# Performance work log

Hardware: AMD Instinct MI355X
Metric: run time of the kernel (lower is better)

## Reference

```python
import math
import jax, jax.numpy as jnp
import numpy as np

IN_FEATURES = 4096
OUT_FEATURES = 4096
BLOCK_SIZE = 256
N_TOKENS = 8192


def _butterfly_layout(out_blocks, in_blocks, butterfly_size):
    # sum of log2(n) butterfly factors with all-ones 2x2 twiddles:
    # block (o, i) is active iff o == i or o == i ^ 2^k for some factor k
    log_n = int(math.log2(butterfly_size))
    idx = np.arange(butterfly_size)
    layout = np.zeros((butterfly_size, butterfly_size), dtype=bool)
    layout[idx, idx] = True
    for k in range(log_n):
        layout[idx ^ (1 << k), idx] = True
    if out_blocks > butterfly_size:
        layout = np.tile(layout, (out_blocks // butterfly_size, 1))
    if in_blocks > butterfly_size:
        layout = np.tile(layout, (1, in_blocks // butterfly_size))
    return layout


def _flat_indices(layout):
    # For each output block, flat indices into [num_in_blocks * active_blocks_per_input]
    # selecting which per-input weight blocks are summed (embedding_bag mode='sum').
    num_out, num_in = layout.shape
    abpi = int(layout.sum(0)[0])
    abpo = int(layout.sum(1)[0])
    rank = np.cumsum(layout, axis=0) - 1  # rank of output o among active outputs of input i
    o_idx, i_idx = np.nonzero(layout)     # row-major -> grouped by output block
    flat = i_idx * abpi + rank[o_idx, i_idx]
    return flat.reshape(num_out, abpo).astype(np.int32), abpi


def setup_inputs() -> dict:
    key = jax.random.key(0)
    k1, k2 = jax.random.split(key)
    in_blocks = IN_FEATURES // BLOCK_SIZE
    out_blocks = OUT_FEATURES // BLOCK_SIZE
    butterfly_size = min(IN_FEATURES, OUT_FEATURES) // BLOCK_SIZE  # 16
    layout = _butterfly_layout(out_blocks, in_blocks, butterfly_size)
    flat_idx, abpi = _flat_indices(layout)  # abpi = log2(16)+1 = 5
    std = math.sqrt(2.0 / (5 * min(IN_FEATURES, OUT_FEATURES)))
    weight = jax.random.normal(k1, (IN_FEATURES, abpi, BLOCK_SIZE), dtype=jnp.float32) * std
    x = jax.random.normal(k2, (N_TOKENS, IN_FEATURES), dtype=jnp.float32)
    return {"x": x, "weight": weight, "flat_indices": jnp.asarray(flat_idx)}


def reference(x, weight, flat_indices):
    # x: [B, in_features]; weight: [in_features, abpi, block_size]
    in_features, abpi, bs = weight.shape
    num_in = in_features // bs
    B = x.shape[0]
    xb = x.reshape(B, num_in, bs)                  # [B, g, k]
    w = weight.reshape(num_in, bs, abpi, bs)       # [g, k, a, o]
    # per-input-block partial output blocks: [g, a, B, o]
    blocks = jnp.einsum('bgk,gkao->gabo', xb, w)
    blocks = blocks.reshape(num_in * abpi, B, bs)
    # gather + sum active blocks per output block (embedding_bag mode='sum')
    out_blocks = blocks[flat_indices].sum(axis=1)  # [num_out_blocks, B, bs]
    out = jnp.transpose(out_blocks, (1, 0, 2)).reshape(B, -1)  # [B, out_features]
    return out
```

## Files before the change

kernel.cpp:

```cpp
#include <hip/hip_runtime.h>
#include <stdint.h>

#define N_TOK 8192
#define IN_F 4096
#define OUT_F 4096
#define BS 256
#define ABPI 5
#define NFLAT 80

typedef __attribute__((ext_vector_type(8))) short short8;
typedef __attribute__((ext_vector_type(4))) float floatx4;
typedef __attribute__((ext_vector_type(4))) unsigned short ushort4v;

__device__ __forceinline__ unsigned short f2bf(float f) {
  union { float f; unsigned int u; } v; v.f = f;
  unsigned int r = v.u + 0x7FFFu + ((v.u >> 16) & 1u);
  return (unsigned short)(r >> 16);
}

__device__ __forceinline__ void async16(const void* g, void* l) {
  __builtin_amdgcn_global_load_lds((const __attribute__((address_space(1))) void*)g,
                                   (__attribute__((address_space(3))) void*)l, 16, 0, 0);
}

__global__ void cvt_x_kernel(const float4* __restrict__ x, ushort4v* __restrict__ xb) {
  int idx = blockIdx.x * 256 + threadIdx.x;
  const int stride = 2048 * 256;
  #pragma unroll
  for (int i = 0; i < 16; ++i, idx += stride) {
    float4 a = x[idx];
    ushort4v o;
    o[0] = f2bf(a.x); o[1] = f2bf(a.y); o[2] = f2bf(a.z); o[3] = f2bf(a.w);
    xb[idx] = o;
  }
}

__global__ void cvt_w_kernel(const float* __restrict__ w, unsigned short* __restrict__ wt) {
  __shared__ unsigned short tile[64][68];
  int b = blockIdx.x;
  int fi = b >> 4;
  int t  = b & 15;
  int k0 = (t >> 2) * 64, o0 = (t & 3) * 64;
  int g = fi / ABPI, a = fi % ABPI;
  int tid = threadIdx.x;
  int tr = tid >> 4, tc = tid & 15;
  #pragma unroll
  for (int i = 0; i < 4; ++i) {
    int k = k0 + i * 16 + tr;
    const float* src = w + (size_t)(g * 256 + k) * (ABPI * BS) + a * BS + o0 + tc * 4;
    float4 v = *(const float4*)src;
    tile[tc * 4 + 0][i * 16 + tr] = f2bf(v.x);
    tile[tc * 4 + 1][i * 16 + tr] = f2bf(v.y);
    tile[tc * 4 + 2][i * 16 + tr] = f2bf(v.z);
    tile[tc * 4 + 3][i * 16 + tr] = f2bf(v.w);
  }
  __syncthreads();
  #pragma unroll
  for (int i = 0; i < 4; ++i) {
    int o = i * 16 + tr;
    unsigned short* dst = wt + (size_t)fi * (BS * BS) + (size_t)(o0 + o) * BS + k0 + tc * 4;
    *(ushort4v*)dst = *(const ushort4v*)&tile[o][tc * 4];
  }
}


#define BM 256
#define BN 256
#define BK 64
#define ABYTES 32768
#define BUFBYTES 65536
#define SMEM_TOTAL 131072

#define SB() __builtin_amdgcn_sched_barrier(0)
#define PRIO1() __builtin_amdgcn_s_setprio(1)
#define PRIO0() __builtin_amdgcn_s_setprio(0)
#define BARRIER() __builtin_amdgcn_s_barrier()
#define LGKM0() do { asm volatile("s_waitcnt lgkmcnt(0)" ::: "memory"); SB(); } while (0)

__device__ __forceinline__ void ld_half_A(const char* p, int c0, int c1, short8 (&af)[4][2]) {
  #pragma unroll
  for (int mt = 0; mt < 4; ++mt) {
    const char* q = p + mt * 2048;
    af[mt][0] = *(const short8*)(q + c0);
    af[mt][1] = *(const short8*)(q + c1);
  }
}

__device__ __forceinline__ void ld_pair_B(const char* p, int c0, int c1, short8 (&bf)[2][2]) {
  #pragma unroll
  for (int nt = 0; nt < 2; ++nt) {
    const char* q = p + nt * 2048;
    bf[nt][0] = *(const short8*)(q + c0);
    bf[nt][1] = *(const short8*)(q + c1);
  }
}

__device__ __forceinline__ void mma16(const short8 (&af)[4][2], const short8 (&bf)[2][2],
                                      floatx4 (&acc)[8][4], int mb, int nb) {
  #pragma unroll
  for (int mt = 0; mt < 4; ++mt)
    #pragma unroll
    for (int nt = 0; nt < 2; ++nt) {
      acc[mb + mt][nb + nt] =
          __builtin_amdgcn_mfma_f32_16x16x32_bf16(af[mt][0], bf[nt][0], acc[mb + mt][nb + nt], 0, 0, 0);
      acc[mb + mt][nb + nt] =
          __builtin_amdgcn_mfma_f32_16x16x32_bf16(af[mt][1], bf[nt][1], acc[mb + mt][nb + nt], 0, 0, 0);
    }
}

#define KTILE(Ab, Bb, Bsd, uB, uA2, STB, STA, END)                              \
  do {                                                                          \
                     \
    if (STB) { async16(pB0 + (uB), (Bsd)         + tid16);                      \
               async16(pB1 + (uB), (Bsd) +  8192 + tid16); }                    \
    ld_half_A((Ab) + rAb,        c0, c1, af);                                   \
    ld_pair_B((Bb) + rBb,        c0, c1, bf01);                                 \
    ld_pair_B((Bb) + rBb + 4096, c0, c1, bf23);                                 \
    SB(); BARRIER(); LGKM0();                                                   \
    PRIO1(); mma16(af, bf01, acc, 0, 0); PRIO0();                               \
    BARRIER();                                                                  \
                                          \
    if (STB) { async16(pB2 + (uB), (Bsd) + 16384 + tid16);                      \
               async16(pB3 + (uB), (Bsd) + 24576 + tid16); }                    \
    SB(); BARRIER();                                                            \
    PRIO1(); mma16(af, bf23, acc, 0, 2); PRIO0();                               \
    BARRIER();                                                                  \
     \
    if (STA) { async16(pA0 + (uA2), (Ab)         + tid16);                      \
               async16(pA2 + (uA2), (Ab) + 16384 + tid16); }                    \
    ld_half_A((Ab) + rAb + 8192, c0, c1, af);                                   \
    SB(); BARRIER(); LGKM0();                                                   \
    PRIO1(); mma16(af, bf23, acc, 4, 2); PRIO0();                               \
    BARRIER();                                                                  \
                                            \
    if (STA) { async16(pA1 + (uA2), (Ab) +  8192 + tid16);                      \
               async16(pA3 + (uA2), (Ab) + 24576 + tid16); }                    \
    SB(); BARRIER();                                                            \
    PRIO1(); mma16(af, bf01, acc, 4, 0); PRIO0();                               \
    if ((END) == 2)      { asm volatile("s_waitcnt vmcnt(4)" ::: "memory");     \
                           SB(); BARRIER(); }                                   \
    else if ((END) == 1) { asm volatile("s_waitcnt vmcnt(0)" ::: "memory");     \
                           SB(); BARRIER(); }                                   \
  } while (0)

__global__ __launch_bounds__(512, 2)
void bfly_gemm(const unsigned short* __restrict__ xb,
               const unsigned short* __restrict__ wt,
               const int* __restrict__ fidx,
               float* __restrict__ out)
{
  extern __shared__ __align__(16) char smem[];
  char* const b0A = smem;
  char* const b0B = b0A + ABYTES;
  char* const b1A = smem + BUFBYTES;
  char* const b1B = b1A + ABYTES;

  const int tid = threadIdx.x;
  const int bx  = blockIdx.x;
  const int swz = (bx & 7) * 64 + (bx >> 3);
  const int ob  = swz >> 5;
  const int mt0 = swz & 31;
  const int m0  = mt0 * BM;
  const int n0g = ob * 256;

  int wbase[ABPI], gcol[ABPI];
  #pragma unroll
  for (int s = 0; s < ABPI; ++s) {
    int fi = __builtin_amdgcn_readfirstlane(fidx[ob * ABPI + s]);
    wbase[s] = fi * (BS * BS);
    gcol[s]  = (fi / ABPI) * BS;
  }

  const int sr = tid >> 3;
  const int sc = tid & 7;
  const int lc = sc ^ (sr & 7);
  const int tid16 = tid * 16;
  const unsigned short* pA0 = xb + (size_t)(m0 +   0 + sr) * IN_F + lc * 8;
  const unsigned short* pA1 = xb + (size_t)(m0 +  64 + sr) * IN_F + lc * 8;
  const unsigned short* pA2 = xb + (size_t)(m0 + 128 + sr) * IN_F + lc * 8;
  const unsigned short* pA3 = xb + (size_t)(m0 + 192 + sr) * IN_F + lc * 8;
  const unsigned short* pB0 = wt + (  0 + sr) * BS + lc * 8;
  const unsigned short* pB1 = wt + ( 64 + sr) * BS + lc * 8;
  const unsigned short* pB2 = wt + (128 + sr) * BS + lc * 8;
  const unsigned short* pB3 = wt + (192 + sr) * BS + lc * 8;

  const int lane = tid & 63;
  const int wv   = tid >> 6;
  const int wm   = (wv >> 2) * 128;
  const int wn   = (wv & 3) * 64;
  const int lrow = lane & 15;
  const int quad = lane >> 4;
  const int rAb  = (wm + lrow) * 128;
  const int rBb  = (wn + lrow) * 128;
  const int c0   = ((quad)     ^ (lrow & 7)) * 16;
  const int c1   = ((quad + 4) ^ (lrow & 7)) * 16;

  short8 af[4][2], bf01[2][2], bf23[2][2];
  floatx4 acc[8][4] = {};

  {
    const int uA0 = gcol[0], uB0 = wbase[0], uA1 = gcol[0] + 64;
    async16(pA0 + uA0, b0A         + tid16);
    async16(pA1 + uA0, b0A +  8192 + tid16);
    async16(pA2 + uA0, b0A + 16384 + tid16);
    async16(pA3 + uA0, b0A + 24576 + tid16);
    async16(pB0 + uB0, b0B         + tid16);
    async16(pB1 + uB0, b0B +  8192 + tid16);
    async16(pB2 + uB0, b0B + 16384 + tid16);
    async16(pB3 + uB0, b0B + 24576 + tid16);
    SB();
    async16(pA0 + uA1, b1A         + tid16);
    async16(pA1 + uA1, b1A +  8192 + tid16);
    async16(pA2 + uA1, b1A + 16384 + tid16);
    async16(pA3 + uA1, b1A + 24576 + tid16);
    asm volatile("s_waitcnt vmcnt(4)" ::: "memory");
    SB();
    BARRIER();
  }

  #pragma unroll 1
  for (int g = 0; g < 4; ++g) {
    const int wbg = wbase[g], gcg = gcol[g];
    const int wbn = wbase[g + 1], gcn = gcol[g + 1];
    KTILE(b0A, b0B, b1B, wbg +  64, gcg + 128, 1, 1, 2);
    KTILE(b1A, b1B, b0B, wbg + 128, gcg + 192, 1, 1, 2);
    KTILE(b0A, b0B, b1B, wbg + 192, gcn,       1, 1, 2);
    KTILE(b1A, b1B, b0B, wbn,       gcn +  64, 1, 1, 2);
  }
  {
    const int wbg = wbase[4], gcg = gcol[4];
    KTILE(b0A, b0B, b1B, wbg +  64, gcg + 128, 1, 1, 2);
    KTILE(b1A, b1B, b0B, wbg + 128, gcg + 192, 1, 1, 2);
    KTILE(b0A, b0B, b1B, wbg + 192, 0,         1, 0, 1);
    KTILE(b1A, b1B, b0B, 0,         0,         0, 0, 0);
  }

  #pragma unroll
  for (int m = 0; m < 8; ++m) {
    const int row = m0 + wm + (m >> 2) * 64 + (m & 3) * 16 + quad * 4;
    #pragma unroll
    for (int n = 0; n < 4; ++n) {
      const int col = n0g + wn + n * 16 + lrow;
      float* po = out + (size_t)row * OUT_F + col;
      #pragma unroll
      for (int r = 0; r < 4; ++r)
        po[(size_t)r * OUT_F] = acc[m][n][r];
    }
  }
}

extern "C" void kernel_launch(void* const* d_in, const int* in_sizes, int n_in,
                              void* d_out, int out_size, void* d_ws, size_t ws_size,
                              hipStream_t stream) {
  const float* x  = (const float*)d_in[0];
  const float* w  = (const float*)d_in[1];
  const int* fidx = (const int*)d_in[2];
  float* out = (float*)d_out;

  unsigned short* xb = (unsigned short*)d_ws;
  unsigned short* wt = xb + (size_t)N_TOK * IN_F;

  static int smem_set = 0;
  if (!smem_set) {
    hipFuncSetAttribute((const void*)bfly_gemm,
                        hipFuncAttributeMaxDynamicSharedMemorySize, SMEM_TOTAL);
    smem_set = 1;
  }

  cvt_x_kernel<<<2048, 256, 0, stream>>>((const float4*)x, (ushort4v*)xb);
  cvt_w_kernel<<<NFLAT * 16, 256, 0, stream>>>(w, wt);
  bfly_gemm<<<16 * 32, 512, SMEM_TOTAL, stream>>>(xb, wt, fidx, out);
}
```

Measured before the change: 328.4 us.

## Fuse fp32-to-bf16 conversion of x into GEMM A-tile loading

Removes the separate cvt_x kernel and its bf16 workspace. The GEMM now loads fp32 x directly through registers, converts it to bf16 and writes it to LDS, interleaved with the MFMA phases, while B still uses async global-to-LDS loads. The goal is to avoid writing and re-reading a 64MB intermediate plus a kernel launch. In exchange, each workgroup reads twice as many A bytes, conversion costs ALU work, and register-staged loads replace async DMA, which adds full vmcnt(0) waits per tile.

New measurement: 396.7 us. 20.8% more time.

```diff
diff --git a/kernel.cpp b/kernel.cpp
--- a/kernel.cpp
+++ b/kernel.cpp
@@ -11,6 +11,7 @@
 typedef __attribute__((ext_vector_type(8))) short short8;
 typedef __attribute__((ext_vector_type(4))) float floatx4;
 typedef __attribute__((ext_vector_type(4))) unsigned short ushort4v;
+typedef __attribute__((ext_vector_type(4))) unsigned int uint4v;
 
 __device__ __forceinline__ unsigned short f2bf(float f) {
   union { float f; unsigned int u; } v; v.f = f;
@@ -21,18 +22,6 @@
 __device__ __forceinline__ void async16(const void* g, void* l) {
   __builtin_amdgcn_global_load_lds((const __attribute__((address_space(1))) void*)g,
                                    (__attribute__((address_space(3))) void*)l, 16, 0, 0);
-}
-
-__global__ void cvt_x_kernel(const float4* __restrict__ x, ushort4v* __restrict__ xb) {
-  int idx = blockIdx.x * 256 + threadIdx.x;
-  const int stride = 2048 * 256;
-  #pragma unroll
-  for (int i = 0; i < 16; ++i, idx += stride) {
-    float4 a = x[idx];
-    ushort4v o;
-    o[0] = f2bf(a.x); o[1] = f2bf(a.y); o[2] = f2bf(a.z); o[3] = f2bf(a.w);
-    xb[idx] = o;
-  }
 }
 
 __global__ void cvt_w_kernel(const float* __restrict__ w, unsigned short* __restrict__ wt) {
@@ -108,43 +97,57 @@
     }
 }
 
-#define KTILE(Ab, Bb, Bsd, uB, uA2, STB, STA, END)                              \
-  do {                                                                          \
-                     \
-    if (STB) { async16(pB0 + (uB), (Bsd)         + tid16);                      \
-               async16(pB1 + (uB), (Bsd) +  8192 + tid16); }                    \
-    ld_half_A((Ab) + rAb,        c0, c1, af);                                   \
-    ld_pair_B((Bb) + rBb,        c0, c1, bf01);                                 \
-    ld_pair_B((Bb) + rBb + 4096, c0, c1, bf23);                                 \
-    SB(); BARRIER(); LGKM0();                                                   \
-    PRIO1(); mma16(af, bf01, acc, 0, 0); PRIO0();                               \
-    BARRIER();                                                                  \
-                                          \
-    if (STB) { async16(pB2 + (uB), (Bsd) + 16384 + tid16);                      \
-               async16(pB3 + (uB), (Bsd) + 24576 + tid16); }                    \
-    SB(); BARRIER();                                                            \
-    PRIO1(); mma16(af, bf23, acc, 0, 2); PRIO0();                               \
-    BARRIER();                                                                  \
-     \
-    if (STA) { async16(pA0 + (uA2), (Ab)         + tid16);                      \
-               async16(pA2 + (uA2), (Ab) + 16384 + tid16); }                    \
-    ld_half_A((Ab) + rAb + 8192, c0, c1, af);                                   \
-    SB(); BARRIER(); LGKM0();                                                   \
-    PRIO1(); mma16(af, bf23, acc, 4, 2); PRIO0();                               \
-    BARRIER();                                                                  \
-                                            \
-    if (STA) { async16(pA1 + (uA2), (Ab) +  8192 + tid16);                      \
-               async16(pA3 + (uA2), (Ab) + 24576 + tid16); }                    \
-    SB(); BARRIER();                                                            \
-    PRIO1(); mma16(af, bf01, acc, 4, 0); PRIO0();                               \
-    if ((END) == 2)      { asm volatile("s_waitcnt vmcnt(4)" ::: "memory");     \
-                           SB(); BARRIER(); }                                   \
-    else if ((END) == 1) { asm volatile("s_waitcnt vmcnt(0)" ::: "memory");     \
-                           SB(); BARRIER(); }                                   \
+#define AQ_ISSUE(q, colA)                                                      \
+  do { const float* p_ = xA + ((q) << 18) + (colA);                            \
+       qa = *(const float4*)p_; qb = *(const float4*)(p_ + 4); } while (0)
+
+#define AQ_WRITE(q, Asd)                                                       \
+  do { uint4v w_;                                                              \
+       w_[0] = (unsigned)f2bf(qa.x) | ((unsigned)f2bf(qa.y) << 16);            \
+       w_[1] = (unsigned)f2bf(qa.z) | ((unsigned)f2bf(qa.w) << 16);            \
+       w_[2] = (unsigned)f2bf(qb.x) | ((unsigned)f2bf(qb.y) << 16);            \
+       w_[3] = (unsigned)f2bf(qb.z) | ((unsigned)f2bf(qb.w) << 16);            \
+       *(uint4v*)((Asd) + (q) * 8192 + tid16) = w_; } while (0)
+
+#define KTILE(Ab, Bb, Asd, Bsd, colA, uB, STAGE)                               \
+  do {                                                                         \
+                       \
+    if (STAGE) AQ_ISSUE(0, colA);                                              \
+    ld_half_A((Ab) + rAb,        c0, c1, af);                                  \
+    ld_pair_B((Bb) + rBb,        c0, c1, bf01);                                \
+    ld_pair_B((Bb) + rBb + 4096, c0, c1, bf23);                                \
+    SB(); BARRIER(); LGKM0();                                                  \
+    PRIO1(); mma16(af, bf01, acc, 0, 0); PRIO0();                              \
+    BARRIER();                                                                 \
+                          \
+    if (STAGE) { AQ_WRITE(0, Asd); AQ_ISSUE(1, colA);                          \
+                 async16(pB0 + (uB), (Bsd)        + tid16);                    \
+                 async16(pB1 + (uB), (Bsd) + 8192 + tid16); }                  \
+    SB(); BARRIER();                                                           \
+    PRIO1(); mma16(af, bf23, acc, 0, 2); PRIO0();                              \
+    BARRIER();                                                                 \
+                \
+    if (STAGE) { AQ_WRITE(1, Asd); AQ_ISSUE(2, colA);                          \
+                 async16(pB2 + (uB), (Bsd) + 16384 + tid16);                   \
+                 async16(pB3 + (uB), (Bsd) + 24576 + tid16); }                 \
+    ld_half_A((Ab) + rAb + 8192, c0, c1, af);                                  \
+    SB(); BARRIER(); LGKM0();                                                  \
+    PRIO1(); mma16(af, bf23, acc, 4, 2); PRIO0();                              \
+    BARRIER();                                                                 \
+       \
+    if (STAGE) { AQ_WRITE(2, Asd); AQ_ISSUE(3, colA); }                        \
+    SB(); BARRIER();                                                           \
+    PRIO1(); mma16(af, bf01, acc, 4, 0); PRIO0();                              \
+    if (STAGE) {                                                               \
+      AQ_WRITE(3, Asd);                                                        \
+      asm volatile("s_waitcnt vmcnt(0)" ::: "memory"); SB();                   \
+      asm volatile("s_waitcnt lgkmcnt(0)" ::: "memory"); SB();                 \
+      BARRIER();                                                               \
+    }                                                                          \
   } while (0)
 
 __global__ __launch_bounds__(512, 2)
-void bfly_gemm(const unsigned short* __restrict__ xb,
+void bfly_gemm(const float* __restrict__ x,
                const unsigned short* __restrict__ wt,
                const int* __restrict__ fidx,
                float* __restrict__ out)
@@ -175,10 +178,7 @@
   const int sc = tid & 7;
   const int lc = sc ^ (sr & 7);
   const int tid16 = tid * 16;
-  const unsigned short* pA0 = xb + (size_t)(m0 +   0 + sr) * IN_F + lc * 8;
-  const unsigned short* pA1 = xb + (size_t)(m0 +  64 + sr) * IN_F + lc * 8;
-  const unsigned short* pA2 = xb + (size_t)(m0 + 128 + sr) * IN_F + lc * 8;
-  const unsigned short* pA3 = xb + (size_t)(m0 + 192 + sr) * IN_F + lc * 8;
+  const float* xA = x + (size_t)(m0 + sr) * IN_F + lc * 8;
   const unsigned short* pB0 = wt + (  0 + sr) * BS + lc * 8;
   const unsigned short* pB1 = wt + ( 64 + sr) * BS + lc * 8;
   const unsigned short* pB2 = wt + (128 + sr) * BS + lc * 8;
@@ -193,28 +193,25 @@
   const int rAb  = (wm + lrow) * 128;
   const int rBb  = (wn + lrow) * 128;
   const int c0   = ((quad)     ^ (lrow & 7)) * 16;
-  const int c1   = ((quad + 4) ^ (lrow & 7)) * 16;
+  const int c1   = c0 ^ 64;
 
   short8 af[4][2], bf01[2][2], bf23[2][2];
+  float4 qa, qb;
   floatx4 acc[8][4] = {};
 
   {
-    const int uA0 = gcol[0], uB0 = wbase[0], uA1 = gcol[0] + 64;
-    async16(pA0 + uA0, b0A         + tid16);
-    async16(pA1 + uA0, b0A +  8192 + tid16);
-    async16(pA2 + uA0, b0A + 16384 + tid16);
-    async16(pA3 + uA0, b0A + 24576 + tid16);
+    const int colA0 = gcol[0], uB0 = wbase[0];
+    #pragma unroll
+    for (int q = 0; q < 4; ++q) {
+      AQ_ISSUE(q, colA0);
+      AQ_WRITE(q, b0A);
+    }
     async16(pB0 + uB0, b0B         + tid16);
     async16(pB1 + uB0, b0B +  8192 + tid16);
     async16(pB2 + uB0, b0B + 16384 + tid16);
     async16(pB3 + uB0, b0B + 24576 + tid16);
-    SB();
-    async16(pA0 + uA1, b1A         + tid16);
-    async16(pA1 + uA1, b1A +  8192 + tid16);
-    async16(pA2 + uA1, b1A + 16384 + tid16);
-    async16(pA3 + uA1, b1A + 24576 + tid16);
-    asm volatile("s_waitcnt vmcnt(4)" ::: "memory");
-    SB();
+    asm volatile("s_waitcnt vmcnt(0)" ::: "memory"); SB();
+    asm volatile("s_waitcnt lgkmcnt(0)" ::: "memory"); SB();
     BARRIER();
   }
 
@@ -222,17 +219,17 @@
   for (int g = 0; g < 4; ++g) {
     const int wbg = wbase[g], gcg = gcol[g];
     const int wbn = wbase[g + 1], gcn = gcol[g + 1];
-    KTILE(b0A, b0B, b1B, wbg +  64, gcg + 128, 1, 1, 2);
-    KTILE(b1A, b1B, b0B, wbg + 128, gcg + 192, 1, 1, 2);
-    KTILE(b0A, b0B, b1B, wbg + 192, gcn,       1, 1, 2);
-    KTILE(b1A, b1B, b0B, wbn,       gcn +  64, 1, 1, 2);
+    KTILE(b0A, b0B, b1A, b1B, gcg +  64, wbg +  64, 1);
+    KTILE(b1A, b1B, b0A, b0B, gcg + 128, wbg + 128, 1);
+    KTILE(b0A, b0B, b1A, b1B, gcg + 192, wbg + 192, 1);
+    KTILE(b1A, b1B, b0A, b0B, gcn,       wbn,       1);
   }
   {
     const int wbg = wbase[4], gcg = gcol[4];
-    KTILE(b0A, b0B, b1B, wbg +  64, gcg + 128, 1, 1, 2);
-    KTILE(b1A, b1B, b0B, wbg + 128, gcg + 192, 1, 1, 2);
-    KTILE(b0A, b0B, b1B, wbg + 192, 0,         1, 0, 1);
-    KTILE(b1A, b1B, b0B, 0,         0,         0, 0, 0);
+    KTILE(b0A, b0B, b1A, b1B, gcg +  64, wbg +  64, 1);
+    KTILE(b1A, b1B, b0A, b0B, gcg + 128, wbg + 128, 1);
+    KTILE(b0A, b0B, b1A, b1B, gcg + 192, wbg + 192, 1);
+    KTILE(b1A, b1B, b0A, b0B, 0,         0,         0);
   }
 
   #pragma unroll
@@ -257,8 +254,7 @@
   const int* fidx = (const int*)d_in[2];
   float* out = (float*)d_out;
 
-  unsigned short* xb = (unsigned short*)d_ws;
-  unsigned short* wt = xb + (size_t)N_TOK * IN_F;
+  unsigned short* wt = (unsigned short*)d_ws;
 
   static int smem_set = 0;
   if (!smem_set) {
@@ -267,7 +263,6 @@
     smem_set = 1;
   }
 
-  cvt_x_kernel<<<2048, 256, 0, stream>>>((const float4*)x, (ushort4v*)xb);
   cvt_w_kernel<<<NFLAT * 16, 256, 0, stream>>>(w, wt);
-  bfly_gemm<<<16 * 32, 512, SMEM_TOTAL, stream>>>(xb, wt, fidx, out);
-}
+  bfly_gemm<<<16 * 32, 512, SMEM_TOTAL, stream>>>(x, wt, fidx, out);
+}
```
